# Kernel optimization log

Hardware: AMD Instinct MI355X
Metric: run time of the kernel (lower is better)

## Reference

```python
import math
import jax, jax.numpy as jnp
import numpy as np

NH = 16          # num_attention_heads
MAX_REL = 512    # max_relative_positions


def _t4(x):
    # [B, N, H] -> [B, NH, N, H/NH]  (transpose_for_scores)
    B, N, H = x.shape
    return x.reshape(B, N, NH, -1).transpose(0, 2, 1, 3)


def setup_inputs() -> dict:
    key = jax.random.key(0)
    ks = jax.random.split(key, 6)
    B, N, H = 1, 2048, 1024
    hidden_states = jax.random.normal(ks[0], (B, N, H), jnp.float32)
    attention_mask = jnp.ones((B, 1, N, N), jnp.int32)
    ids = jnp.arange(N, dtype=jnp.int32)
    relative_pos = ids[:, None] - ids[None, :]              # [N, N], build_relative_position
    rel_embeddings = jax.random.normal(ks[1], (2 * MAX_REL, H), jnp.float32) * 0.02
    in_proj_w = jax.random.normal(ks[2], (3 * H, H), jnp.float32) * 0.02
    q_bias = jnp.zeros((H,), jnp.float32)
    v_bias = jnp.zeros((H,), jnp.float32)
    pos_proj_w = jax.random.normal(ks[3], (H, H), jnp.float32) * 0.02
    pos_q_proj_w = jax.random.normal(ks[4], (H, H), jnp.float32) * 0.02
    pos_q_proj_b = jnp.zeros((H,), jnp.float32)
    return dict(hidden_states=hidden_states, attention_mask=attention_mask,
                relative_pos=relative_pos, rel_embeddings=rel_embeddings,
                in_proj_w=in_proj_w, q_bias=q_bias, v_bias=v_bias,
                pos_proj_w=pos_proj_w, pos_q_proj_w=pos_q_proj_w,
                pos_q_proj_b=pos_q_proj_b)


def reference(hidden_states, attention_mask, relative_pos, rel_embeddings,
              in_proj_w, q_bias, v_bias, pos_proj_w, pos_q_proj_w, pos_q_proj_b):
    B, N, H = hidden_states.shape
    dh = H // NH
    scale_factor = 1 + 2  # 1 + len(["c2p", "p2c"])
    scale = math.sqrt(dh * scale_factor)

    # fused QKV projection; chunk(3, dim=-1) AFTER transpose_for_scores -> per-head q|k|v layout
    qp = hidden_states @ in_proj_w.T                          # [B, N, 3H]
    q, k, v = jnp.split(_t4(qp), 3, axis=-1)                  # each [B, NH, N, dh]
    q = q + _t4(q_bias[None, None, :])
    v = v + _t4(v_bias[None, None, :])
    q = q / scale

    scores = jnp.einsum('bhqd,bhkd->bhqk', q, k)              # content-content

    # disentangled relative-position bias
    span = min(N, MAX_REL)                                    # att_span
    rel = rel_embeddings[MAX_REL - span:MAX_REL + span][None] # [1, 2S, H]
    rpos = relative_pos.astype(jnp.int32)[None, None]         # [1, 1, N, N]

    # c2p: content-to-position
    pos_k = _t4(rel @ pos_proj_w.T)                           # [1, NH, 2S, dh]
    c2p = jnp.einsum('bhqd,xhsd->bhqs', q, pos_k)             # [B, NH, N, 2S]
    c2p_pos = jnp.clip(rpos + span, 0, 2 * span - 1)
    c2p = jnp.take_along_axis(c2p, c2p_pos, axis=-1)          # gather -> [B, NH, N, N]

    # p2c: position-to-content
    pos_q = _t4(rel @ pos_q_proj_w.T + pos_q_proj_b) / scale  # [1, NH, 2S, dh]
    p2c = jnp.einsum('bhkd,xhsd->bhks', k, pos_q)             # [B, NH, N, 2S]
    p2c_pos = jnp.clip(-rpos + span, 0, 2 * span - 1)
    p2c = jnp.take_along_axis(p2c, p2c_pos, axis=-1)          # [B, NH, K, Q]
    p2c = jnp.swapaxes(p2c, -1, -2)                           # -> [B, NH, Q, K]

    scores = scores + c2p + p2c

    # XSoftmax: masked softmax, masked probs zeroed
    m = attention_mask.astype(bool)                           # [B, 1, N, N]
    probs = jax.nn.softmax(jnp.where(m, scores, -jnp.inf), axis=-1)
    probs = jnp.where(m, probs, 0.0)

    ctx = jnp.einsum('bhqk,bhkd->bhqd', probs, v)             # [B, NH, N, dh]
    return ctx.transpose(0, 2, 1, 3).reshape(B, N, H)
```

## Files before the change

### kernel.cpp

```cpp
#include <hip/hip_runtime.h>
#include <hip/hip_bf16.h>

typedef __bf16 bf16;
typedef __attribute__((ext_vector_type(8))) __bf16 bf16x8;
typedef __attribute__((ext_vector_type(8))) float f32x8;
typedef __attribute__((ext_vector_type(4))) float f32x4;

#define MFMA(a,b,c) __builtin_amdgcn_mfma_f32_16x16x32_bf16((a),(b),(c),0,0,0)

__device__ __forceinline__ bf16x8 ld8(const bf16* p){ bf16x8 v; __builtin_memcpy(&v,p,16); return v; }
__device__ __forceinline__ void   st8(bf16* p, bf16x8 v){ __builtin_memcpy(p,&v,16); }

__global__ __launch_bounds__(256)
void cvt_kernel(const float* __restrict__ s0, const float* __restrict__ s1,
                const float* __restrict__ s2, const float* __restrict__ s3,
                const float* __restrict__ s4,
                bf16* d0, bf16* d1, bf16* d2, bf16* d3, bf16* d4)
{
    const int sizes[5] = {2097152, 3145728, 1048576, 1048576, 1048576};
    const float* s; bf16* d;
    switch (blockIdx.y) {
        case 0: s = s0; d = d0; break;  case 1: s = s1; d = d1; break;
        case 2: s = s2; d = d2; break;  case 3: s = s3; d = d3; break;
        default: s = s4; d = d4;
    }
    const int n = sizes[blockIdx.y];
    const int stride = gridDim.x * 256 * 8;
    for (int i = (blockIdx.x * 256 + threadIdx.x) * 8; i < n; i += stride) {
        f32x8 v; __builtin_memcpy(&v, s + i, 32);
        bf16x8 r;
        #pragma unroll
        for (int j = 0; j < 8; j++) r[j] = (bf16)v[j];
        st8(d + i, r);
    }
}

__global__ __launch_bounds__(256)
void gemm_stage(const bf16* __restrict__ A, const bf16* __restrict__ Bpk,
                const bf16* __restrict__ Bpq, int K, int mode,
                const float* __restrict__ qb, const float* __restrict__ vb,
                bf16* __restrict__ o0, bf16* __restrict__ o1, bf16* __restrict__ o2,
                float* __restrict__ part)
{
    __shared__ __attribute__((aligned(16))) bf16 As[128][32];
    __shared__ __attribute__((aligned(16))) bf16 Bs[128][32];

    const int tid = threadIdx.x, w = tid >> 6, lane = tid & 63;
    const int l15 = lane & 15, quad = lane >> 4;
    const int wr = w >> 1, wc = w & 1;

    int arr = 0, my = blockIdx.y, kbeg = 0, kend = K;
    const bf16* B = Bpk;
    if (mode == 1) {
        arr = my >> 3; my &= 7;
        B = arr ? Bpq : Bpk;
        kbeg = blockIdx.z * 256; kend = kbeg + 256;
    }
    const int m0 = my * 128, n0 = blockIdx.x * 128;
    const int srow = tid >> 2, scol = (tid & 3) * 8;

    f32x4 acc[4][4] = {};
    for (int k0 = kbeg; k0 < kend; k0 += 32) {
        __syncthreads();
        st8(&As[srow][scol],    ld8(A + (size_t)(m0 + srow) * K + k0 + scol));
        st8(&As[srow+64][scol], ld8(A + (size_t)(m0 + 64 + srow) * K + k0 + scol));
        st8(&Bs[srow][scol],    ld8(B + (size_t)(n0 + srow) * K + k0 + scol));
        st8(&Bs[srow+64][scol], ld8(B + (size_t)(n0 + 64 + srow) * K + k0 + scol));
        __syncthreads();
        bf16x8 a[4], b[4];
        #pragma unroll
        for (int i = 0; i < 4; i++) a[i] = ld8(&As[wr*64 + i*16 + l15][quad*8]);
        #pragma unroll
        for (int j = 0; j < 4; j++) b[j] = ld8(&Bs[wc*64 + j*16 + l15][quad*8]);
        #pragma unroll
        for (int i = 0; i < 4; i++)
            #pragma unroll
            for (int j = 0; j < 4; j++)
                acc[i][j] = MFMA(a[i], b[j], acc[i][j]);
    }

    const float inv_scale = 0.07216878364870323f;
    #pragma unroll
    for (int i = 0; i < 4; i++) {
        #pragma unroll
        for (int j = 0; j < 4; j++) {
            #pragma unroll
            for (int r = 0; r < 4; r++) {
                int row = m0 + wr*64 + i*16 + quad*4 + r;
                int col = n0 + wc*64 + j*16 + l15;
                float v = acc[i][j][r];
                if (mode == 0) {
                    int h = col / 192, rr = col % 192;
                    if (rr < 64)
                        o0[((size_t)h*2048 + row)*64 + rr] =
                            (bf16)((v + qb[h*64 + rr]) * inv_scale);
                    else if (rr < 128)
                        o1[((size_t)h*2048 + row)*64 + (rr - 64)] = (bf16)v;
                    else
                        o2[((size_t)h*64 + (rr - 128))*2048 + row] =
                            (bf16)(v + vb[h*64 + (rr - 128)]);
                } else {
                    part[(((size_t)(arr*4 + blockIdx.z)*1024 + row)*1024) + col] = v;
                }
            }
        }
    }
}

__global__ __launch_bounds__(256)
void pos_merge(const float* __restrict__ part, const float* __restrict__ pqb,
               bf16* __restrict__ PKw, bf16* __restrict__ PQw)
{
    int e = blockIdx.x * 256 + threadIdx.x;
    int arr = e >> 20, r = (e >> 10) & 1023, c = e & 1023;
    const float* p = part + ((size_t)arr*4) * 1048576 + (size_t)r * 1024 + c;
    float v = p[0] + p[1048576] + p[2*1048576] + p[3*1048576];
    int h = c >> 6, d = c & 63;
    if (arr == 0) PKw[((size_t)h*1024 + r)*64 + d] = (bf16)v;
    else          PQw[((size_t)h*1024 + r)*64 + d] =
                      (bf16)((v + pqb[c]) * 0.07216878364870323f);
}

__global__ __launch_bounds__(256)
void edge_kernel(const bf16* __restrict__ Qw, const bf16* __restrict__ Kw,
                 const bf16* __restrict__ PKw, const bf16* __restrict__ PQw,
                 float* __restrict__ C2Pe, float* __restrict__ P2Ce)
{
    int t = blockIdx.x * 256 + threadIdx.x;
    int side = t >> 15, rest = t & 32767;
    int h = rest >> 11, n = rest & 2047;
    const bf16* row = (side ? Kw : Qw) + ((size_t)h*2048 + n) * 64;
    const bf16* eb  = (side ? PQw : PKw) + (size_t)h*1024*64;
    float a0 = 0.f, a1 = 0.f;
    #pragma unroll
    for (int c = 0; c < 8; c++) {
        bf16x8 x  = ld8(row + c*8);
        bf16x8 e0 = ld8(eb + c*8);
        bf16x8 e1 = ld8(eb + (size_t)1023*64 + c*8);
        #pragma unroll
        for (int j = 0; j < 8; j++) {
            a0 += (float)x[j] * (float)e0[j];
            a1 += (float)x[j] * (float)e1[j];
        }
    }
    float* o = side ? P2Ce : C2Pe;
    o[((size_t)h*2048 + n)*2 + 0] = a0;
    o[((size_t)h*2048 + n)*2 + 1] = a1;
}

__global__ __launch_bounds__(64, 2)
void attn_kernel(const bf16* __restrict__ Q, const bf16* __restrict__ Kc,
                 const bf16* __restrict__ Vt, const bf16* __restrict__ PK,
                 const bf16* __restrict__ PQ,
                 const float* __restrict__ C2Pe, const float* __restrict__ P2Ce,
                 float* __restrict__ out)
{
    __shared__ bf16 W1s[16][82];
    __shared__ bf16 W2s[64][82];
    __shared__ __attribute__((aligned(16))) bf16 Ps[16][72];

    const int lane = threadIdx.x;
    const int l15 = lane & 15, quad = lane >> 4;
    const int h = blockIdx.y, qw0 = blockIdx.x * 16;

    const bf16* Qh  = Q  + (size_t)h * 2048 * 64;
    const bf16* Kh  = Kc + (size_t)h * 2048 * 64;
    const bf16* Vh  = Vt + (size_t)h * 64 * 2048;
    const bf16* PKh = PK + (size_t)h * 1024 * 64;
    const bf16* PQh = PQ + (size_t)h * 1024 * 64;

    bf16x8 qa[2];
    #pragma unroll
    for (int s = 0; s < 2; s++)
        qa[s] = ld8(Qh + (size_t)(qw0 + l15)*64 + s*32 + quad*8);

    float c2pe0[4], c2pe1[4];
    #pragma unroll
    for (int r = 0; r < 4; r++) {
        int q = qw0 + quad*4 + r;
        c2pe0[r] = C2Pe[((size_t)h*2048 + q)*2 + 0];
        c2pe1[r] = C2Pe[((size_t)h*2048 + q)*2 + 1];
    }

    f32x4 oacc[4] = {};
    float psum[4] = {0.f, 0.f, 0.f, 0.f};

    for (int kb = 0; kb < 32; kb++) {
        const int k0 = kb * 64;

        bf16x8 kf[4][2];
        #pragma unroll
        for (int nt = 0; nt < 4; nt++)
            #pragma unroll
            for (int s = 0; s < 2; s++)
                kf[nt][s] = ld8(Kh + (size_t)(k0 + nt*16 + l15)*64 + s*32 + quad*8);

        f32x4 sacc[4] = {};
        #pragma unroll
        for (int s = 0; s < 2; s++)
            #pragma unroll
            for (int nt = 0; nt < 4; nt++)
                sacc[nt] = MFMA(qa[s], kf[nt][s], sacc[nt]);

        float val[4][4];
        if (k0 >= qw0 + 527) {
            float p2[4];
            #pragma unroll
            for (int nt = 0; nt < 4; nt++)
                p2[nt] = P2Ce[((size_t)h*2048 + k0 + nt*16 + l15)*2 + 0];
            #pragma unroll
            for (int nt = 0; nt < 4; nt++)
                #pragma unroll
                for (int r = 0; r < 4; r++)
                    val[nt][r] = sacc[nt][r] + c2pe0[r] + p2[nt];
        } else if (k0 <= qw0 - 574) {
            float p2[4];
            #pragma unroll
            for (int nt = 0; nt < 4; nt++)
                p2[nt] = P2Ce[((size_t)h*2048 + k0 + nt*16 + l15)*2 + 1];
            #pragma unroll
            for (int nt = 0; nt < 4; nt++)
                #pragma unroll
                for (int r = 0; r < 4; r++)
                    val[nt][r] = sacc[nt][r] + c2pe1[r] + p2[nt];
        } else {
            const int winb = qw0 - k0 + 449;
            {
                f32x4 a1[5] = {};
                #pragma unroll
                for (int s = 0; s < 2; s++)
                    #pragma unroll
                    for (int n5 = 0; n5 < 5; n5++) {
                        int c = winb + n5*16 + l15;
                        c = min(max(c, 0), 1023);
                        bf16x8 bq = ld8(PKh + (size_t)c*64 + s*32 + quad*8);
                        a1[n5] = MFMA(qa[s], bq, a1[n5]);
                    }
                #pragma unroll
                for (int n5 = 0; n5 < 5; n5++)
                    #pragma unroll
                    for (int r = 0; r < 4; r++)
                        W1s[quad*4 + r][n5*16 + l15] = (bf16)a1[n5][r];
            }
            {
                bf16x8 pq[5][2];
                #pragma unroll
                for (int s = 0; s < 2; s++)
                    #pragma unroll
                    for (int n5 = 0; n5 < 5; n5++) {
                        int c = winb + n5*16 + l15;
                        c = min(max(c, 0), 1023);
                        pq[n5][s] = ld8(PQh + (size_t)c*64 + s*32 + quad*8);
                    }
                #pragma unroll
                for (int mt = 0; mt < 4; mt++) {
                    f32x4 a2[5] = {};
                    #pragma unroll
                    for (int s = 0; s < 2; s++)
                        #pragma unroll
                        for (int n5 = 0; n5 < 5; n5++)
                            a2[n5] = MFMA(kf[mt][s], pq[n5][s], a2[n5]);
                    #pragma unroll
                    for (int n5 = 0; n5 < 5; n5++)
                        #pragma unroll
                        for (int r = 0; r < 4; r++)
                            W2s[mt*16 + quad*4 + r][n5*16 + l15] = (bf16)a2[n5][r];
                }
            }
            #pragma unroll
            for (int nt = 0; nt < 4; nt++)
                #pragma unroll
                for (int r = 0; r < 4; r++) {
                    int off = quad*4 + r - nt*16 - l15 + 63;
                    val[nt][r] = sacc[nt][r] + (float)W1s[quad*4 + r][off]
                                             + (float)W2s[nt*16 + l15][off];
                }
        }

        #pragma unroll
        for (int nt = 0; nt < 4; nt++)
            #pragma unroll
            for (int r = 0; r < 4; r++) {
                float e = __expf(val[nt][r]);
                psum[r] += e;
                Ps[quad*4 + r][nt*16 + l15] = (bf16)e;
            }

        #pragma unroll
        for (int s = 0; s < 2; s++) {
            bf16x8 pa = ld8(&Ps[l15][s*32 + quad*8]);
            #pragma unroll
            for (int dt = 0; dt < 4; dt++) {
                bf16x8 vf = ld8(Vh + (size_t)(dt*16 + l15)*2048 + k0 + s*32 + quad*8);
                oacc[dt] = MFMA(pa, vf, oacc[dt]);
            }
        }
    }

    #pragma unroll
    for (int r = 0; r < 4; r++)
        #pragma unroll
        for (int m = 1; m < 16; m <<= 1)
            psum[r] += __shfl_xor(psum[r], m);
    #pragma unroll
    for (int dt = 0; dt < 4; dt++)
        #pragma unroll
        for (int r = 0; r < 4; r++) {
            int row = qw0 + quad*4 + r;
            out[(size_t)row*1024 + h*64 + dt*16 + l15] = oacc[dt][r] / psum[r];
        }
}

extern "C" void kernel_launch(void* const* d_in, const int* in_sizes, int n_in,
                              void* d_out, int out_size, void* d_ws, size_t ws_size,
                              hipStream_t stream)
{
    (void)in_sizes; (void)n_in; (void)out_size; (void)ws_size;
    const float* X   = (const float*)d_in[0];
    const float* REL = (const float*)d_in[3];
    const float* Win = (const float*)d_in[4];
    const float* qb  = (const float*)d_in[5];
    const float* vb  = (const float*)d_in[6];
    const float* Wpk = (const float*)d_in[7];
    const float* Wpq = (const float*)d_in[8];
    const float* pqb = (const float*)d_in[9];
    float* out = (float*)d_out;

    char* ws = (char*)d_ws;
    const size_t MB = 1024u * 1024u;
    bf16*  Xb    = (bf16*)(ws);
    bf16*  Winb  = (bf16*)(ws + 4*MB);
    bf16*  Wpkb  = (bf16*)(ws + 10*MB);
    bf16*  Wpqb  = (bf16*)(ws + 12*MB);
    bf16*  RELb  = (bf16*)(ws + 14*MB);
    bf16*  Qw    = (bf16*)(ws + 16*MB);
    bf16*  Kw    = (bf16*)(ws + 20*MB);
    bf16*  Vtw   = (bf16*)(ws + 24*MB);
    bf16*  PKw   = (bf16*)(ws + 28*MB);
    bf16*  PQw   = (bf16*)(ws + 30*MB);
    float* Ppart = (float*)(ws + 32*MB);
    float* C2Pe  = (float*)(ws + 64*MB);
    float* P2Ce  = (float*)(ws + 64*MB + 256*1024);

    cvt_kernel<<<dim3(1536, 5), 256, 0, stream>>>(X, Win, Wpk, Wpq, REL,
                                                  Xb, Winb, Wpkb, Wpqb, RELb);
    gemm_stage<<<dim3(24, 16, 1), 256, 0, stream>>>(Xb, Winb, Winb, 1024, 0,
                                                    qb, vb, Qw, Kw, Vtw, nullptr);
    gemm_stage<<<dim3(8, 16, 4), 256, 0, stream>>>(RELb, Wpkb, Wpqb, 1024, 1,
                                                   nullptr, nullptr,
                                                   nullptr, nullptr, nullptr, Ppart);
    pos_merge<<<dim3(8192), 256, 0, stream>>>(Ppart, pqb, PKw, PQw);
    edge_kernel<<<dim3(256), 256, 0, stream>>>(Qw, Kw, PKw, PQw, C2Pe, P2Ce);
    attn_kernel<<<dim3(128, 16), 64, 0, stream>>>(Qw, Kw, Vtw, PKw, PQw,
                                                  C2Pe, P2Ce, out);
}
```

Before: 369.5 us.

## Split attention over key blocks across grid z and merge partial sums

The attention kernel now splits the 32 key blocks across four grid-z slices, interleaved, and writes unnormalized partial outputs and row sums to workspace. A new merge kernel adds the partials and divides. The W2 shared buffer shrinks to a double-buffered 16-row tile consumed per mt, which cuts LDS use and allows a higher occupancy hint. The goal is more blocks in flight (2048 waves was low for the device), at the cost of extra partial-result traffic and an added launch. The workspace regions are reused: Ppart space holds Opart and the RELb space holds PSpart.

Result: slower. 457.3 us (+23.8%).

```diff
diff --git a/kernel.cpp b/kernel.cpp
--- a/kernel.cpp
+++ b/kernel.cpp
@@ -148,20 +148,22 @@
     o[((size_t)h*2048 + n)*2 + 1] = a1;
 }
 
-__global__ __launch_bounds__(64, 2)
+#define KSPLIT 4
+
+__global__ __launch_bounds__(64, 4)
 void attn_kernel(const bf16* __restrict__ Q, const bf16* __restrict__ Kc,
                  const bf16* __restrict__ Vt, const bf16* __restrict__ PK,
                  const bf16* __restrict__ PQ,
                  const float* __restrict__ C2Pe, const float* __restrict__ P2Ce,
-                 float* __restrict__ out)
+                 float* __restrict__ opart, float* __restrict__ pspart)
 {
     __shared__ bf16 W1s[16][82];
-    __shared__ bf16 W2s[64][82];
+    __shared__ bf16 W2s[2][16][82];
     __shared__ __attribute__((aligned(16))) bf16 Ps[16][72];
 
     const int lane = threadIdx.x;
     const int l15 = lane & 15, quad = lane >> 4;
-    const int h = blockIdx.y, qw0 = blockIdx.x * 16;
+    const int h = blockIdx.y, qw0 = blockIdx.x * 16, z = blockIdx.z;
 
     const bf16* Qh  = Q  + (size_t)h * 2048 * 64;
     const bf16* Kh  = Kc + (size_t)h * 2048 * 64;
@@ -185,7 +187,8 @@
     f32x4 oacc[4] = {};
     float psum[4] = {0.f, 0.f, 0.f, 0.f};
 
-    for (int kb = 0; kb < 32; kb++) {
+    for (int i = 0; i < 32 / KSPLIT; i++) {
+        const int kb = z + i * KSPLIT;
         const int k0 = kb * 64;
 
         bf16x8 kf[4][2];
@@ -264,17 +267,15 @@
                     for (int n5 = 0; n5 < 5; n5++)
                         #pragma unroll
                         for (int r = 0; r < 4; r++)
-                            W2s[mt*16 + quad*4 + r][n5*16 + l15] = (bf16)a2[n5][r];
+                            W2s[mt & 1][quad*4 + r][n5*16 + l15] = (bf16)a2[n5][r];
+                    #pragma unroll
+                    for (int r = 0; r < 4; r++) {
+                        int off = quad*4 + r - mt*16 - l15 + 63;
+                        val[mt][r] = sacc[mt][r] + (float)W1s[quad*4 + r][off]
+                                                 + (float)W2s[mt & 1][l15][off];
+                    }
                 }
             }
-            #pragma unroll
-            for (int nt = 0; nt < 4; nt++)
-                #pragma unroll
-                for (int r = 0; r < 4; r++) {
-                    int off = quad*4 + r - nt*16 - l15 + 63;
-                    val[nt][r] = sacc[nt][r] + (float)W1s[quad*4 + r][off]
-                                             + (float)W2s[nt*16 + l15][off];
-                }
         }
 
         #pragma unroll
@@ -302,13 +303,36 @@
         #pragma unroll
         for (int m = 1; m < 16; m <<= 1)
             psum[r] += __shfl_xor(psum[r], m);
+
+    const size_t zb = (size_t)(z * 16 + h);
     #pragma unroll
     for (int dt = 0; dt < 4; dt++)
         #pragma unroll
         for (int r = 0; r < 4; r++) {
             int row = qw0 + quad*4 + r;
-            out[(size_t)row*1024 + h*64 + dt*16 + l15] = oacc[dt][r] / psum[r];
-        }
+            opart[(zb*2048 + row)*64 + dt*16 + l15] = oacc[dt][r];
+        }
+    if (l15 == 0) {
+        #pragma unroll
+        for (int r = 0; r < 4; r++)
+            pspart[zb*2048 + qw0 + quad*4 + r] = psum[r];
+    }
+}
+
+__global__ __launch_bounds__(256)
+void attn_merge(const float* __restrict__ opart, const float* __restrict__ pspart,
+                float* __restrict__ out)
+{
+    int t = blockIdx.x * 256 + threadIdx.x;
+    int row = t >> 10, c = t & 1023, h = c >> 6, d = c & 63;
+    float o = 0.f, p = 0.f;
+    #pragma unroll
+    for (int zz = 0; zz < KSPLIT; zz++) {
+        size_t zb = (size_t)(zz * 16 + h);
+        o += opart[(zb*2048 + row)*64 + d];
+        p += pspart[zb*2048 + row];
+    }
+    out[t] = o / p;
 }
 
 extern "C" void kernel_launch(void* const* d_in, const int* in_sizes, int n_in,
@@ -341,6 +365,8 @@
     float* Ppart = (float*)(ws + 32*MB);
     float* C2Pe  = (float*)(ws + 64*MB);
     float* P2Ce  = (float*)(ws + 64*MB + 256*1024);
+    float* Opart  = (float*)(ws + 32*MB);
+    float* PSpart = (float*)(ws + 14*MB);
 
     cvt_kernel<<<dim3(1536, 5), 256, 0, stream>>>(X, Win, Wpk, Wpq, REL,
                                                   Xb, Winb, Wpkb, Wpqb, RELb);
@@ -351,6 +377,7 @@
                                                    nullptr, nullptr, nullptr, Ppart);
     pos_merge<<<dim3(8192), 256, 0, stream>>>(Ppart, pqb, PKw, PQw);
     edge_kernel<<<dim3(256), 256, 0, stream>>>(Qw, Kw, PKw, PQw, C2Pe, P2Ce);
-    attn_kernel<<<dim3(128, 16), 64, 0, stream>>>(Qw, Kw, Vtw, PKw, PQw,
-                                                  C2Pe, P2Ce, out);
-}
+    attn_kernel<<<dim3(128, 16, KSPLIT), 64, 0, stream>>>(Qw, Kw, Vtw, PKw, PQw,
+                                                          C2Pe, P2Ce, Opart, PSpart);
+    attn_merge<<<dim3(8192), 256, 0, stream>>>(Opart, PSpart, out);
+}
```
